# Optimization experiments

Measured on AMD Instinct MI355X. Metric: run time of the kernel, lower is better.

Reference implementation:

```python
import jax, jax.numpy as jnp
import numpy as np

WS = 7  # window size of the inner WindowAttention
EPS = 1e-5


def pc_roll(xb, shifts, axis):
    """Per-channel circular roll of [B,C,H,W] along `axis` (2 or 3).
    torch.roll semantics: out[i] = in[(i - shift) % n]."""
    n = xb.shape[axis]
    idx = (jnp.arange(n)[None, :] - shifts[:, None]) % n  # [C, n]
    if axis == 2:
        idxb = jnp.broadcast_to(idx[None, :, :, None], xb.shape)
    else:
        idxb = jnp.broadcast_to(idx[None, :, None, :], xb.shape)
    return jnp.take_along_axis(xb, idxb, axis=axis)


def layernorm(x, w, b):
    m = x.mean(-1, keepdims=True)
    v = x.var(-1, keepdims=True)
    return (x - m) * jax.lax.rsqrt(v + EPS) * w + b


def batchnorm2d(x, g, b):
    # training-mode BN: batch statistics over (B,H,W) per channel
    m = x.mean(axis=(0, 2, 3), keepdims=True)
    v = x.var(axis=(0, 2, 3), keepdims=True)
    return (x - m) * jax.lax.rsqrt(v + EPS) * g[None, :, None, None] + b[None, :, None, None]


def conv1x1(x, w, b):
    # x: [B,C,H,W], w: [Cout,Cin]
    return jnp.einsum('bchw,oc->bohw', x, w) + b[None, :, None, None]


def window_attention(q, k, v):
    # single-head Swin-style window attention, 7x7 windows, no rel-pos bias
    B, C, H, W = q.shape
    nh, nw = H // WS, W // WS

    def part(t):  # [B,C,H,W] -> [B*nh*nw, WS*WS, C]
        t = t.reshape(B, C, nh, WS, nw, WS)
        return t.transpose(0, 2, 4, 3, 5, 1).reshape(B * nh * nw, WS * WS, C)

    qw, kw, vw = part(q), part(k), part(v)
    scale = C ** -0.5
    attn = jax.nn.softmax(jnp.einsum('wnc,wmc->wnm', qw, kw) * scale, axis=-1)
    out = jnp.einsum('wnm,wmc->wnc', attn, vw)
    out = out.reshape(B, nh, nw, WS, WS, C).transpose(0, 5, 1, 3, 2, 4).reshape(B, C, H, W)
    return out


def setup_inputs() -> dict:
    B, H, W, C = 32, 56, 56, 128
    N = H * W
    key = jax.random.key(0)
    ks = jax.random.split(key, 16)
    f32 = jnp.float32

    def lin_w(k, din, dout):
        return 0.02 * jax.random.normal(k, (din, dout), dtype=f32)

    conv_std = float(np.sqrt(2.0 / C))
    inp = {
        'x': jax.random.normal(ks[0], (B, N, C), dtype=f32),
        'fc1_w': lin_w(ks[1], C, C), 'fc1_b': jnp.zeros((C,), f32),
        'fc2_w': lin_w(ks[2], C, C), 'fc2_b': jnp.zeros((C,), f32),
        'fc3_w': lin_w(ks[3], C, C), 'fc3_b': jnp.zeros((C,), f32),
        'fc4_w': lin_w(ks[4], C, C), 'fc4_b': jnp.zeros((C,), f32),
        'fc5_w': lin_w(ks[5], 2 * C, C), 'fc5_b': jnp.zeros((C,), f32),
        'fc6_w': lin_w(ks[6], 2 * C, C), 'fc6_b': jnp.zeros((C,), f32),
        'ln_w': jnp.ones((2 * C,), f32), 'ln_b': jnp.zeros((2 * C,), f32),
        'q_w': conv_std * jax.random.normal(ks[7], (C, C), dtype=f32), 'q_b': jnp.zeros((C,), f32),
        'k_w': conv_std * jax.random.normal(ks[8], (C, C), dtype=f32), 'k_b': jnp.zeros((C,), f32),
        'v_w': conv_std * jax.random.normal(ks[9], (C, C), dtype=f32), 'v_b': jnp.zeros((C,), f32),
        'bn1_g': jnp.ones((C,), f32), 'bn1_b': jnp.zeros((C,), f32),
        'bn2_g': jnp.ones((C,), f32), 'bn2_b': jnp.zeros((C,), f32),
        'H': H, 'W': W,
    }
    return inp


def reference(x, fc1_w, fc1_b, fc2_w, fc2_b, fc3_w, fc3_b, fc4_w, fc4_b,
              fc5_w, fc5_b, fc6_w, fc6_b, ln_w, ln_b,
              q_w, q_b, k_w, k_b, v_w, v_b, bn1_g, bn1_b, bn2_g, bn2_b, H, W):
    B, N, C = x.shape
    shifts = jnp.arange(C)
    gelu = lambda t: jax.nn.gelu(t, approximate=False)

    def to_bchw(t):
        return t.transpose(0, 2, 1).reshape(B, C, H, W)

    def to_bnc(t):
        return t.reshape(B, C, N).transpose(0, 2, 1)

    # branch 1: roll +c along H -> fc1 -> GELU -> roll +c along W -> fc2
    h = to_bnc(pc_roll(to_bchw(x), shifts, axis=2))
    h = gelu(h @ fc1_w + fc1_b)
    h = to_bnc(pc_roll(to_bchw(h), shifts, axis=3))
    x_1 = h @ fc2_w + fc2_b

    # branch 2: roll -c along W -> fc3 -> GELU -> roll +c along H -> fc4
    h = to_bnc(pc_roll(to_bchw(x), -shifts, axis=3))
    h = gelu(h @ fc3_w + fc3_b)
    h = to_bnc(pc_roll(to_bchw(h), shifts, axis=2))
    x_2 = h @ fc4_w + fc4_b

    x_1 = x_1 + x
    x_2 = x_2 + x
    x1 = jnp.concatenate([x_1, x_2], axis=2)          # [B,N,2C]
    x1 = layernorm(x1, ln_w, ln_b)
    x1 = x1 @ fc5_w + fc5_b
    x1 = x1 + x

    # local-attention branch (DWConv module actually runs WindowAtten + BN + ReLU)
    xb = to_bchw(x)
    att = window_attention(conv1x1(xb, q_w, q_b), conv1x1(xb, k_w, k_b), conv1x1(xb, v_w, v_b))
    x2 = jax.nn.relu(batchnorm2d(att, bn1_g, bn1_b))  # DWConv forward
    x2 = jax.nn.relu(x2)                              # act2 (idempotent, kept for fidelity)
    x2 = batchnorm2d(x2, bn2_g, bn2_b)                # norm2
    x2 = x2.reshape(B, C, N).transpose(0, 2, 1)       # [B,N,C]

    x3 = jnp.concatenate([x1, x2], axis=2)            # [B,N,2C]
    return x3 @ fc6_w + fc6_b
```

## Files before the change

### kernel.cpp

```cpp
#include <hip/hip_runtime.h>
#include <hip/hip_bf16.h>
#include <cstdint>
#include <cstddef>

typedef __bf16 bf16_t;
typedef __bf16 bf16x8 __attribute__((ext_vector_type(8)));
typedef float f32x4 __attribute__((ext_vector_type(4)));

#define B_SZ 32
#define H_SZ 56
#define W_SZ 56
#define N_TOK 3136
#define CH 128
#define M_TOT 100352

#define WOFF_FC1 0
#define WOFF_FC2 16384
#define WOFF_FC3 32768
#define WOFF_FC4 49152
#define WOFF_FC5 65536
#define WOFF_FC6 98304
#define WOFF_QW  131072
#define WOFF_KW  147456
#define WOFF_VW  163840
#define WTOT     180224

enum { A_FLAT = 0, A_WROLL, A_LN, A_BN };
enum { E_BIAS = 0, E_GELU, E_RES };

__device__ __forceinline__ float bf2f(bf16_t v) { return (float)v; }
__device__ __forceinline__ unsigned short bfbits(float v) {
    bf16_t b = (bf16_t)v; unsigned short u; __builtin_memcpy(&u, &b, 2); return u;
}

__global__ __launch_bounds__(256)
void wcvt_k(const float* __restrict__ f1, const float* __restrict__ f2,
            const float* __restrict__ f3, const float* __restrict__ f4,
            const float* __restrict__ f5, const float* __restrict__ f6,
            const float* __restrict__ qw, const float* __restrict__ kw,
            const float* __restrict__ vw, bf16_t* __restrict__ wb)
{
    const int blk = blockIdx.x;
    const int tid = threadIdx.x;
    if (blk < 32) {
        __shared__ bf16_t T[64][72];
        const float* src; bf16_t* dst; int K, t;
        if (blk < 4)       { src = f1; dst = wb + WOFF_FC1; K = 128; t = blk; }
        else if (blk < 8)  { src = f2; dst = wb + WOFF_FC2; K = 128; t = blk - 4; }
        else if (blk < 12) { src = f3; dst = wb + WOFF_FC3; K = 128; t = blk - 8; }
        else if (blk < 16) { src = f4; dst = wb + WOFF_FC4; K = 128; t = blk - 12; }
        else if (blk < 24) { src = f5; dst = wb + WOFF_FC5; K = 256; t = blk - 16; }
        else               { src = f6; dst = wb + WOFF_FC6; K = 256; t = blk - 24; }
        const int ti = t >> 1;
        const int tj = t & 1;
        for (int it = tid; it < 64 * 16; it += 256) {
            const int r = it >> 4, c4 = it & 15;
            float4 u = *(const float4*)(src + (size_t)(ti * 64 + r) * 128 + tj * 64 + c4 * 4);
            T[c4 * 4 + 0][r] = (bf16_t)u.x;
            T[c4 * 4 + 1][r] = (bf16_t)u.y;
            T[c4 * 4 + 2][r] = (bf16_t)u.z;
            T[c4 * 4 + 3][r] = (bf16_t)u.w;
        }
        __syncthreads();
        for (int it = tid; it < 64 * 8; it += 256) {
            const int n = it >> 3, ck = it & 7;
            *(uint4*)(dst + (size_t)(tj * 64 + n) * K + ti * 64 + ck * 8) =
                *(const uint4*)(&T[n][ck * 8]);
        }
    } else {
        const float* src; bf16_t* dst;
        int t = blk - 32;
        if (t < 4)      { src = qw; dst = wb + WOFF_QW; }
        else if (t < 8) { src = kw; dst = wb + WOFF_KW; t -= 4; }
        else            { src = vw; dst = wb + WOFF_VW; t -= 8; }
        const int base = t * 4096 + tid * 16;
        float4 u0 = *(const float4*)(src + base);
        float4 u1 = *(const float4*)(src + base + 4);
        float4 u2 = *(const float4*)(src + base + 8);
        float4 u3 = *(const float4*)(src + base + 12);
        bf16_t o[16] = {(bf16_t)u0.x, (bf16_t)u0.y, (bf16_t)u0.z, (bf16_t)u0.w,
                        (bf16_t)u1.x, (bf16_t)u1.y, (bf16_t)u1.z, (bf16_t)u1.w,
                        (bf16_t)u2.x, (bf16_t)u2.y, (bf16_t)u2.z, (bf16_t)u2.w,
                        (bf16_t)u3.x, (bf16_t)u3.y, (bf16_t)u3.z, (bf16_t)u3.w};
        *(uint4*)(dst + base) = *(const uint4*)o;
        *(uint4*)(dst + base + 8) = *(const uint4*)(o + 8);
    }
}

__global__ __launch_bounds__(256)
void transpose_k(const float* __restrict__ x, bf16_t* __restrict__ xT)
{
    __shared__ bf16_t T[128][70];
    const int tid = threadIdx.x;
    const int mbase = blockIdx.x * 64;
    const int bimg = mbase / N_TOK;
    const int n0 = mbase - bimg * N_TOK;
    for (int idx = tid; idx < 64 * 32; idx += 256) {
        const int tok = idx >> 5, cg = idx & 31;
        float4 u = *(const float4*)(x + (size_t)(mbase + tok) * CH + cg * 4);
        T[cg * 4 + 0][tok] = (bf16_t)u.x;
        T[cg * 4 + 1][tok] = (bf16_t)u.y;
        T[cg * 4 + 2][tok] = (bf16_t)u.z;
        T[cg * 4 + 3][tok] = (bf16_t)u.w;
    }
    __syncthreads();
    const uint* T32 = (const uint*)&T[0][0];
    for (int idx = tid; idx < 128 * 8; idx += 256) {
        const int c = idx >> 3, chunk = idx & 7;
        uint4 o;
        o.x = T32[c * 35 + chunk * 4 + 0];
        o.y = T32[c * 35 + chunk * 4 + 1];
        o.z = T32[c * 35 + chunk * 4 + 2];
        o.w = T32[c * 35 + chunk * 4 + 3];
        *(uint4*)(xT + ((size_t)(bimg * 128 + c)) * N_TOK + n0 + chunk * 8) = o;
    }
}

template<int AMODE, int KHALVES, int EPI, int WDIR, int OTRANS, int OF32>
__global__ __launch_bounds__(256)
void gemm_k(const bf16_t* __restrict__ A0, const bf16_t* __restrict__ A1,
            const bf16_t* __restrict__ Wt, const float* __restrict__ bias,
            const float* __restrict__ resid,
            const float* __restrict__ rowst,
            const float* __restrict__ lnw, const float* __restrict__ lnb,
            const float* __restrict__ bnp,
            void* __restrict__ outv)
{
    __shared__ __align__(16) char smem[17920];
    bf16_t* As = (bf16_t*)smem;
    const int tid = threadIdx.x;
    const int mbase = blockIdx.x * 64;
    const int bimg = mbase / N_TOK;
    const int n0 = mbase - bimg * N_TOK;
    const int lane = tid & 63;
    const int wv = tid >> 6;
    const int qd = lane >> 4;
    const int mr = lane & 15;
    const int KS = 128 * KHALVES;

    f32x4 acc[4][2];
#pragma unroll
    for (int i = 0; i < 4; ++i)
#pragma unroll
        for (int j = 0; j < 2; ++j) { f32x4 z = {0.f,0.f,0.f,0.f}; acc[i][j] = z; }

    for (int kh = 0; kh < KHALVES; ++kh) {
        if (kh) __syncthreads();
        if (AMODE == A_FLAT || AMODE == A_WROLL) {
            for (int idx = tid; idx < 128 * 8; idx += 256) {
                const int c = idx >> 3, chunk = idx & 7;
                const int cm = (c >= 112) ? c - 112 : (c >= 56 ? c - 56 : c);
                const bf16_t* crow = A0 + ((size_t)(bimg * 128 + c)) * N_TOK;
                if (AMODE == A_FLAT) {
                    int t = n0 + chunk * 8 + N_TOK - 56 * cm;
                    if (t >= N_TOK) t -= N_TOK;
                    uint4 u = *(const uint4*)(crow + t);
                    const bf16_t* up = (const bf16_t*)&u;
#pragma unroll
                    for (int j = 0; j < 8; ++j) As[(chunk * 8 + j) * 136 + c] = up[j];
                } else {
                    const int nl = n0 + chunk * 8;
                    const int h = nl / 56;
                    const int w0 = nl - h * 56;
                    int ws = (WDIR > 0) ? (w0 + cm) : (w0 + 56 - cm);
                    if (ws >= 56) ws -= 56;
                    const bf16_t* hrow = crow + h * 56;
                    if (ws <= 48) {
                        uint4 u = *(const uint4*)(hrow + ws);
                        const bf16_t* up = (const bf16_t*)&u;
#pragma unroll
                        for (int j = 0; j < 8; ++j) As[(chunk * 8 + j) * 136 + c] = up[j];
                    } else {
#pragma unroll
                        for (int j = 0; j < 8; ++j) {
                            int wj = ws + j; if (wj >= 56) wj -= 56;
                            As[(chunk * 8 + j) * 136 + c] = hrow[wj];
                        }
                    }
                }
            }
        } else if (AMODE == A_LN) {
            for (int idx = tid; idx < 64 * 16; idx += 256) {
                const int row = idx >> 4, ck = idx & 15;
                const int rowg = mbase + row;
                const bf16_t* src = kh ? A1 : A0;
                uint4 u = *(const uint4*)(src + (size_t)rowg * CH + ck * 8);
                const bf16_t* up = (const bf16_t*)&u;
                const float mean = rowst[2 * rowg];
                const float rstd = rowst[2 * rowg + 1];
                const int cabs = kh * 128 + ck * 8;
                bf16_t t[8];
#pragma unroll
                for (int j = 0; j < 8; ++j) {
                    float v = (bf2f(up[j]) - mean) * rstd;
                    v = v * lnw[cabs + j] + lnb[cabs + j];
                    t[j] = (bf16_t)v;
                }
                *(uint4*)(&As[row * 136 + ck * 8]) = *(const uint4*)t;
            }
        } else {
            for (int idx = tid; idx < 64 * 16; idx += 256) {
                const int row = idx >> 4, ck = idx & 15;
                const int rowg = mbase + row;
                if (kh == 0) {
                    uint4 u = *(const uint4*)(A0 + (size_t)rowg * CH + ck * 8);
                    *(uint4*)(&As[row * 136 + ck * 8]) = u;
                } else {
                    uint4 u = *(const uint4*)(A1 + (size_t)rowg * CH + ck * 8);
                    const bf16_t* up = (const bf16_t*)&u;
                    bf16_t t[8];
#pragma unroll
                    for (int j = 0; j < 8; ++j) {
                        const int c = ck * 8 + j;
                        float z = fmaxf(0.f, bf2f(up[j]) * bnp[c] + bnp[128 + c]);
                        t[j] = (bf16_t)(z * bnp[256 + c] + bnp[384 + c]);
                    }
                    *(uint4*)(&As[row * 136 + ck * 8]) = *(const uint4*)t;
                }
            }
        }
        __syncthreads();
        const bf16_t* wbase = Wt + (size_t)(wv * 32 + mr) * KS + kh * 128 + qd * 8;
        bf16x8 bfr[4][2];
#pragma unroll
        for (int kt = 0; kt < 4; ++kt)
#pragma unroll
            for (int nt = 0; nt < 2; ++nt)
                bfr[kt][nt] = *(const bf16x8*)(wbase + (size_t)(nt * 16) * KS + kt * 32);
#pragma unroll
        for (int kt = 0; kt < 4; ++kt) {
            bf16x8 af[4];
#pragma unroll
            for (int mt = 0; mt < 4; ++mt)
                af[mt] = *(const bf16x8*)(&As[(mt * 16 + mr) * 136 + kt * 32 + qd * 8]);
#pragma unroll
            for (int mt = 0; mt < 4; ++mt)
#pragma unroll
                for (int nt = 0; nt < 2; ++nt)
                    acc[mt][nt] = __builtin_amdgcn_mfma_f32_16x16x32_bf16(
                        af[mt], bfr[kt][nt], acc[mt][nt], 0, 0, 0);
        }
    }
    if (OTRANS) {
        __syncthreads();
        uint* T32 = (uint*)smem;
#pragma unroll
        for (int mt = 0; mt < 4; ++mt)
#pragma unroll
            for (int nt = 0; nt < 2; ++nt) {
                const int col = wv * 32 + nt * 16 + mr;
                const float bb = bias[col];
#pragma unroll
                for (int rp = 0; rp < 2; ++rp) {
                    float v0 = acc[mt][nt][2 * rp] + bb;
                    float v1 = acc[mt][nt][2 * rp + 1] + bb;
                    if (EPI == E_GELU) {
                        v0 = 0.5f * v0 * (1.f + erff(v0 * 0.70710678118654752f));
                        v1 = 0.5f * v1 * (1.f + erff(v1 * 0.70710678118654752f));
                    }
                    T32[col * 35 + mt * 8 + qd * 2 + rp] =
                        (uint)bfbits(v0) | ((uint)bfbits(v1) << 16);
                }
            }
        __syncthreads();
        const int c = tid >> 1, half = tid & 1;
        uint r[16];
#pragma unroll
        for (int j = 0; j < 16; ++j) r[j] = T32[c * 35 + half * 16 + j];
        bf16_t* op = (bf16_t*)outv + ((size_t)(bimg * 128 + c)) * N_TOK + n0 + half * 32;
        uint4 o0 = {r[0], r[1], r[2], r[3]};
        uint4 o1 = {r[4], r[5], r[6], r[7]};
        uint4 o2 = {r[8], r[9], r[10], r[11]};
        uint4 o3 = {r[12], r[13], r[14], r[15]};
        ((uint4*)op)[0] = o0; ((uint4*)op)[1] = o1;
        ((uint4*)op)[2] = o2; ((uint4*)op)[3] = o3;
    } else {
#pragma unroll
        for (int mt = 0; mt < 4; ++mt)
#pragma unroll
            for (int nt = 0; nt < 2; ++nt) {
                const int col = wv * 32 + nt * 16 + mr;
                const float bb = bias[col];
#pragma unroll
                for (int r = 0; r < 4; ++r) {
                    const int rowg = mbase + mt * 16 + qd * 4 + r;
                    float v = acc[mt][nt][r] + bb;
                    if (EPI == E_GELU) v = 0.5f * v * (1.f + erff(v * 0.70710678118654752f));
                    if (EPI == E_RES)  v += resid[(size_t)rowg * CH + col];
                    if (OF32) ((float*)outv)[(size_t)rowg * CH + col] = v;
                    else ((bf16_t*)outv)[(size_t)rowg * CH + col] = (bf16_t)v;
                }
            }
    }
}

__global__ __launch_bounds__(256)
void qkv_k(const float* __restrict__ x, const bf16_t* __restrict__ wb,
           const float* __restrict__ qb, const float* __restrict__ kb,
           const float* __restrict__ vb,
           bf16_t* __restrict__ qo, bf16_t* __restrict__ ko, bf16_t* __restrict__ vo)
{
    __shared__ __align__(16) bf16_t As[64 * 136];
    const int tid = threadIdx.x;
    const int mbase = blockIdx.x * 64;
    const int lane = tid & 63;
    const int wv = tid >> 6;
    const int qd = lane >> 4;
    const int mr = lane & 15;

    for (int idx = tid; idx < 64 * 16; idx += 256) {
        const int row = idx >> 4, ck = idx & 15;
        const float* p = x + (size_t)(mbase + row) * CH + ck * 8;
        float4 u0 = *(const float4*)p;
        float4 u1 = *(const float4*)(p + 4);
        bf16_t t[8] = {(bf16_t)u0.x, (bf16_t)u0.y, (bf16_t)u0.z, (bf16_t)u0.w,
                       (bf16_t)u1.x, (bf16_t)u1.y, (bf16_t)u1.z, (bf16_t)u1.w};
        *(uint4*)(&As[row * 136 + ck * 8]) = *(const uint4*)t;
    }
    __syncthreads();
    bf16x8 af[4][4];
#pragma unroll
    for (int kt = 0; kt < 4; ++kt)
#pragma unroll
        for (int mt = 0; mt < 4; ++mt)
            af[kt][mt] = *(const bf16x8*)(&As[(mt * 16 + mr) * 136 + kt * 32 + qd * 8]);

    const int woffs[3] = {WOFF_QW, WOFF_KW, WOFF_VW};
    const float* bs3[3] = {qb, kb, vb};
    bf16_t* os3[3] = {qo, ko, vo};
#pragma unroll
    for (int s = 0; s < 3; ++s) {
        const bf16_t* wbase = wb + woffs[s] + (size_t)(wv * 32 + mr) * 128 + qd * 8;
        f32x4 acc[4][2];
#pragma unroll
        for (int i = 0; i < 4; ++i)
#pragma unroll
            for (int j = 0; j < 2; ++j) { f32x4 z = {0.f,0.f,0.f,0.f}; acc[i][j] = z; }
#pragma unroll
        for (int kt = 0; kt < 4; ++kt) {
            bf16x8 bfr[2];
#pragma unroll
            for (int nt = 0; nt < 2; ++nt)
                bfr[nt] = *(const bf16x8*)(wbase + (nt * 16) * 128 + kt * 32);
#pragma unroll
            for (int mt = 0; mt < 4; ++mt)
#pragma unroll
                for (int nt = 0; nt < 2; ++nt)
                    acc[mt][nt] = __builtin_amdgcn_mfma_f32_16x16x32_bf16(
                        af[kt][mt], bfr[nt], acc[mt][nt], 0, 0, 0);
        }
        bf16_t* out = os3[s];
#pragma unroll
        for (int mt = 0; mt < 4; ++mt)
#pragma unroll
            for (int nt = 0; nt < 2; ++nt) {
                const int col = wv * 32 + nt * 16 + mr;
                const float bb = bs3[s][col];
#pragma unroll
                for (int r = 0; r < 4; ++r) {
                    const int rowg = mbase + mt * 16 + qd * 4 + r;
                    out[(size_t)rowg * CH + col] = (bf16_t)(acc[mt][nt][r] + bb);
                }
            }
    }
}

__global__ __launch_bounds__(256)
void rowstats_k(const bf16_t* __restrict__ x1p, const bf16_t* __restrict__ x2p,
                float* __restrict__ rs)
{
    const int row = blockIdx.x * 4 + (threadIdx.x >> 6);
    const int lane = threadIdx.x & 63;
    const bf16_t* p1 = x1p + (size_t)row * CH + lane * 2;
    const bf16_t* p2 = x2p + (size_t)row * CH + lane * 2;
    float a0 = bf2f(p1[0]), a1 = bf2f(p1[1]);
    float b0 = bf2f(p2[0]), b1 = bf2f(p2[1]);
    float s = a0 + a1 + b0 + b1;
    float sq = a0 * a0 + a1 * a1 + b0 * b0 + b1 * b1;
#pragma unroll
    for (int off = 32; off > 0; off >>= 1) {
        s += __shfl_down(s, off);
        sq += __shfl_down(sq, off);
    }
    if (lane == 0) {
        float mean = s * (1.f / 256.f);
        float var = sq * (1.f / 256.f) - mean * mean;
        rs[2 * row] = mean;
        rs[2 * row + 1] = rsqrtf(var + 1e-5f);
    }
}

__global__ __launch_bounds__(256, 6)
void attn_k(const bf16_t* __restrict__ qg, const bf16_t* __restrict__ kg,
            const bf16_t* __restrict__ vg, bf16_t* __restrict__ og,
            float* __restrict__ partial)
{
    __shared__ __align__(16) char smem[27136];
    bf16_t* Kr = (bf16_t*)smem;
    bf16_t* Vt = (bf16_t*)smem;
    bf16_t* Ps = (bf16_t*)(smem + 17408);
    float* bnacc = (float*)(smem + 26112);
    bf16_t* Os = (bf16_t*)smem;

    const int tid = threadIdx.x;
    const int blk = blockIdx.x;
    const int b = blk >> 6;
    const int wy = (blk >> 3) & 7;
    const int wx = blk & 7;
    const int lane = tid & 63;
    const int wv = tid >> 6;
    const int qd = lane >> 4;
    const int mr = lane & 15;

    bnacc[tid] = 0.f;

    const int kck = tid & 15;
    const int kt0 = tid >> 4;
    uint4 kld[4];
#pragma unroll
    for (int it = 0; it < 4; ++it) {
        const int i = kt0 + it * 16;
        uint4 u = {0, 0, 0, 0};
        if (i < 49) {
            const int n = (wy * 7 + i / 7) * 56 + wx * 7 + (i % 7);
            u = *(const uint4*)(kg + ((size_t)b * N_TOK + n) * CH + kck * 8);
        }
        kld[it] = u;
    }

    const int vi0 = tid & 15;
    const int vck = tid >> 4;
    uint4 vld[4];
#pragma unroll
    for (int it = 0; it < 4; ++it) {
        const int i = vi0 + it * 16;
        uint4 uv = {0, 0, 0, 0};
        if (i < 49) {
            const int n = (wy * 7 + i / 7) * 56 + wx * 7 + (i % 7);
            uv = *(const uint4*)(vg + ((size_t)b * N_TOK + n) * CH + vck * 8);
        }
        vld[it] = uv;
    }

    const int qrow = wv * 16 + mr;
    const int qc = qrow < 49 ? qrow : 48;
    const bf16_t* qptr = qg + ((size_t)b * N_TOK +
                               (wy * 7 + qc / 7) * 56 + wx * 7 + (qc % 7)) * CH + qd * 8;
    bf16x8 aq[4];
#pragma unroll
    for (int kt = 0; kt < 4; ++kt)
        aq[kt] = *(const bf16x8*)(qptr + kt * 32);

#pragma unroll
    for (int it = 0; it < 4; ++it)
        *(uint4*)(&Kr[(kt0 + it * 16) * 132 + kck * 8]) = kld[it];
    __syncthreads();

    f32x4 sacc[4];
#pragma unroll
    for (int nt = 0; nt < 4; ++nt) {
        f32x4 a = {0.f, 0.f, 0.f, 0.f};
#pragma unroll
        for (int kt = 0; kt < 4; ++kt) {
            bf16x8 bk = *(const bf16x8*)(&Kr[(nt * 16 + mr) * 132 + kt * 32 + qd * 8]);
            a = __builtin_amdgcn_mfma_f32_16x16x32_bf16(aq[kt], bk, a, 0, 0, 0);
        }
        sacc[nt] = a;
    }

    float pv[4][4];
    float inv[4];
    {
        const float SCALE = 0.088388347648318447f;
#pragma unroll
        for (int nt = 0; nt < 4; ++nt) {
            const bool bad = (nt * 16 + mr) > 48;
#pragma unroll
            for (int r = 0; r < 4; ++r)
                sacc[nt][r] = bad ? -1e30f : sacc[nt][r] * SCALE;
        }
#pragma unroll
        for (int r = 0; r < 4; ++r) {
            float m = fmaxf(fmaxf(sacc[0][r], sacc[1][r]), fmaxf(sacc[2][r], sacc[3][r]));
            m = fmaxf(m, __shfl_xor(m, 1));
            m = fmaxf(m, __shfl_xor(m, 2));
            m = fmaxf(m, __shfl_xor(m, 4));
            m = fmaxf(m, __shfl_xor(m, 8));
#pragma unroll
            for (int nt = 0; nt < 4; ++nt) pv[nt][r] = __expf(sacc[nt][r] - m);
            float s = (pv[0][r] + pv[1][r]) + (pv[2][r] + pv[3][r]);
            s += __shfl_xor(s, 1);
            s += __shfl_xor(s, 2);
            s += __shfl_xor(s, 4);
            s += __shfl_xor(s, 8);
            inv[r] = 1.f / s;
        }
    }
    __syncthreads();

#pragma unroll
    for (int it = 0; it < 4; ++it) {
        const int i = vi0 + it * 16;
        const bf16_t* vp = (const bf16_t*)&vld[it];
#pragma unroll
        for (int j = 0; j < 8; ++j)
            Vt[(vck * 8 + j) * 68 + i] = vp[j];
    }
#pragma unroll
    for (int nt = 0; nt < 4; ++nt)
#pragma unroll
        for (int r = 0; r < 4; ++r)
            Ps[(wv * 16 + qd * 4 + r) * 68 + nt * 16 + mr] = (bf16_t)(pv[nt][r] * inv[r]);
    __syncthreads();

    bf16x8 ap[2];
    ap[0] = *(const bf16x8*)(&Ps[(wv * 16 + mr) * 68 + qd * 8]);
    ap[1] = *(const bf16x8*)(&Ps[(wv * 16 + mr) * 68 + 32 + qd * 8]);
    f32x4 oacc[8];
#pragma unroll
    for (int nt = 0; nt < 8; ++nt) {
        f32x4 a = {0.f, 0.f, 0.f, 0.f};
#pragma unroll
        for (int kt = 0; kt < 2; ++kt) {
            bf16x8 bv = *(const bf16x8*)(&Vt[(nt * 16 + mr) * 68 + kt * 32 + qd * 8]);
            a = __builtin_amdgcn_mfma_f32_16x16x32_bf16(ap[kt], bv, a, 0, 0, 0);
        }
        oacc[nt] = a;
    }

#pragma unroll
    for (int nt = 0; nt < 8; ++nt) {
        const int c = nt * 16 + mr;
        float s = 0.f, sq = 0.f;
#pragma unroll
        for (int r = 0; r < 4; ++r) {
            const int q = wv * 16 + qd * 4 + r;
            if (q < 49) { const float v = oacc[nt][r]; s += v; sq += v * v; }
        }
        s += __shfl_xor(s, 16); sq += __shfl_xor(sq, 16);
        s += __shfl_xor(s, 32); sq += __shfl_xor(sq, 32);
        if (qd == 0) { atomicAdd(&bnacc[c], s); atomicAdd(&bnacc[128 + c], sq); }
    }
    __syncthreads();

#pragma unroll
    for (int nt = 0; nt < 8; ++nt) {
        const int c = nt * 16 + mr;
#pragma unroll
        for (int r = 0; r < 4; ++r) {
            const int q = wv * 16 + qd * 4 + r;
            Os[q * 136 + c] = (bf16_t)oacc[nt][r];
        }
    }
    __syncthreads();

    for (int idx = tid; idx < 49 * 16; idx += 256) {
        const int row = idx >> 4, u = idx & 15;
        const int n = (wy * 7 + row / 7) * 56 + wx * 7 + (row % 7);
        *(uint4*)(og + ((size_t)b * N_TOK + n) * CH + u * 8) =
            *(const uint4*)(&Os[row * 136 + u * 8]);
    }
    partial[(size_t)blk * 256 + tid] = bnacc[tid];
}

__global__ __launch_bounds__(256)
void bnreduce_k(const float* __restrict__ partial, float* __restrict__ accum)
{
    const int t = threadIdx.x;
    const int r0 = blockIdx.x * 16;
    float s = 0.f;
#pragma unroll
    for (int r = 0; r < 16; ++r) s += partial[(size_t)(r0 + r) * 256 + t];
    atomicAdd(&accum[t], s);
}

__global__ __launch_bounds__(256)
void bnstats2_k(const bf16_t* __restrict__ att, const float* __restrict__ g1,
                const float* __restrict__ b1, float* __restrict__ accum)
{
    __shared__ float ls[256], lq[256];
    const int c = threadIdx.x & 127;
    const int half = threadIdx.x >> 7;
    const float m = accum[c] * (1.f / (float)M_TOT);
    const float var = accum[128 + c] * (1.f / (float)M_TOT) - m * m;
    const float rstd = rsqrtf(var + 1e-5f);
    const float scl = g1[c] * rstd;
    const float sh = b1[c] - m * scl;
    const size_t rowbase = (size_t)blockIdx.x * 196;
    float s = 0.f, sq = 0.f;
    for (int r = half; r < 196; r += 2) {
        float z = fmaxf(0.f, bf2f(att[(rowbase + r) * CH + c]) * scl + sh);
        s += z; sq += z * z;
    }
    ls[threadIdx.x] = s; lq[threadIdx.x] = sq;
    __syncthreads();
    if (threadIdx.x < 128) {
        atomicAdd(&accum[256 + c], ls[threadIdx.x] + ls[threadIdx.x + 128]);
        atomicAdd(&accum[384 + c], lq[threadIdx.x] + lq[threadIdx.x + 128]);
    }
}

__global__ void bnparams_k(const float* __restrict__ accum,
                           const float* __restrict__ g1, const float* __restrict__ b1,
                           const float* __restrict__ g2, const float* __restrict__ b2,
                           float* __restrict__ bnp)
{
    const int c = threadIdx.x;
    const float inv = 1.f / (float)M_TOT;
    float m1 = accum[c] * inv;
    float v1 = accum[128 + c] * inv - m1 * m1;
    float rs1 = rsqrtf(v1 + 1e-5f);
    float s1 = g1[c] * rs1;
    float sh1 = b1[c] - m1 * s1;
    float m2 = accum[256 + c] * inv;
    float v2 = accum[384 + c] * inv - m2 * m2;
    float rs2 = rsqrtf(v2 + 1e-5f);
    float s2 = g2[c] * rs2;
    float sh2 = b2[c] - m2 * s2;
    bnp[c] = s1; bnp[128 + c] = sh1; bnp[256 + c] = s2; bnp[384 + c] = sh2;
}

__global__ void zero_k(float* __restrict__ p) { p[threadIdx.x] = 0.f; }

extern "C" void kernel_launch(void* const* d_in, const int* in_sizes, int n_in,
                              void* d_out, int out_size, void* d_ws, size_t ws_size,
                              hipStream_t stream)
{
    (void)in_sizes; (void)n_in; (void)out_size; (void)ws_size;
    const float* x     = (const float*)d_in[0];
    const float* fc1_w = (const float*)d_in[1];
    const float* fc1_b = (const float*)d_in[2];
    const float* fc2_w = (const float*)d_in[3];
    const float* fc2_b = (const float*)d_in[4];
    const float* fc3_w = (const float*)d_in[5];
    const float* fc3_b = (const float*)d_in[6];
    const float* fc4_w = (const float*)d_in[7];
    const float* fc4_b = (const float*)d_in[8];
    const float* fc5_w = (const float*)d_in[9];
    const float* fc5_b = (const float*)d_in[10];
    const float* fc6_w = (const float*)d_in[11];
    const float* fc6_b = (const float*)d_in[12];
    const float* ln_w  = (const float*)d_in[13];
    const float* ln_b  = (const float*)d_in[14];
    const float* q_w   = (const float*)d_in[15];
    const float* q_b   = (const float*)d_in[16];
    const float* k_w   = (const float*)d_in[17];
    const float* k_b   = (const float*)d_in[18];
    const float* v_w   = (const float*)d_in[19];
    const float* v_b   = (const float*)d_in[20];
    const float* bn1_g = (const float*)d_in[21];
    const float* bn1_b = (const float*)d_in[22];
    const float* bn2_g = (const float*)d_in[23];
    const float* bn2_b = (const float*)d_in[24];

    char* ws = (char*)d_ws;
    const size_t SZB = (size_t)M_TOT * CH * sizeof(bf16_t);
    bf16_t* bufA = (bf16_t*)(ws);
    bf16_t* bufB = (bf16_t*)(ws + SZB);
    bf16_t* bufC = (bf16_t*)(ws + 2 * SZB);
    bf16_t* bufD = (bf16_t*)(ws + 3 * SZB);
    float*  rs   = (float*)(ws + 4 * SZB);
    float*  accum = (float*)(ws + 4 * SZB + (size_t)M_TOT * 2 * sizeof(float));
    float*  bnp  = accum + 512;
    float*  partial = bnp + 512;
    bf16_t* wbuf = (bf16_t*)(partial + 2048 * 256);

    const dim3 blk(256);
    const int GG = M_TOT / 64;

    zero_k<<<1, 512, 0, stream>>>(accum);
    wcvt_k<<<44, blk, 0, stream>>>(fc1_w, fc2_w, fc3_w, fc4_w, fc5_w, fc6_w,
                                   q_w, k_w, v_w, wbuf);
    transpose_k<<<GG, blk, 0, stream>>>(x, bufA);
    gemm_k<A_FLAT, 1, E_GELU, 0, 1, 0><<<GG, blk, 0, stream>>>(
        bufA, nullptr, wbuf + WOFF_FC1, fc1_b, nullptr, nullptr, nullptr, nullptr, nullptr, bufB);
    gemm_k<A_WROLL, 1, E_RES, -1, 0, 0><<<GG, blk, 0, stream>>>(
        bufB, nullptr, wbuf + WOFF_FC2, fc2_b, x, nullptr, nullptr, nullptr, nullptr, bufC);
    gemm_k<A_WROLL, 1, E_GELU, 1, 1, 0><<<GG, blk, 0, stream>>>(
        bufA, nullptr, wbuf + WOFF_FC3, fc3_b, nullptr, nullptr, nullptr, nullptr, nullptr, bufB);
    gemm_k<A_FLAT, 1, E_RES, 0, 0, 0><<<GG, blk, 0, stream>>>(
        bufB, nullptr, wbuf + WOFF_FC4, fc4_b, x, nullptr, nullptr, nullptr, nullptr, bufD);
    rowstats_k<<<M_TOT / 4, blk, 0, stream>>>(bufC, bufD, rs);
    gemm_k<A_LN, 2, E_RES, 0, 0, 0><<<GG, blk, 0, stream>>>(
        bufC, bufD, wbuf + WOFF_FC5, fc5_b, x, rs, ln_w, ln_b, nullptr, bufB);
    qkv_k<<<GG, blk, 0, stream>>>(x, wbuf, q_b, k_b, v_b, bufA, bufC, bufD);
    attn_k<<<B_SZ * 64, blk, 0, stream>>>(bufA, bufC, bufD, bufA, partial);
    bnreduce_k<<<128, blk, 0, stream>>>(partial, accum);
    bnstats2_k<<<512, blk, 0, stream>>>(bufA, bn1_g, bn1_b, accum);
    bnparams_k<<<1, 128, 0, stream>>>(accum, bn1_g, bn1_b, bn2_g, bn2_b, bnp);
    gemm_k<A_BN, 2, E_BIAS, 0, 0, 1><<<GG, blk, 0, stream>>>(
        bufB, bufA, wbuf + WOFF_FC6, fc6_b, nullptr, nullptr, nullptr, nullptr, bnp, d_out);
}
```

Baseline: 467.1 us.

## Fuse fc1 and fc2 branch into one row kernel; read K directly in attention

Adds a kernel that handles one image row per block: it gathers the H-rolled input from the transposed buffer, runs fc1 with GELU into shared memory, applies the per-channel W-roll inside shared memory, then runs fc2 with bias and residual. This replaces two GEMM launches and the intermediate bufB round-trip through global memory. Separately, the attention kernel now loads K fragments straight from global memory instead of staging them in LDS, which removes one barrier and lets the V transpose overlap the softmax. The trade-off is higher LDS use per block and K loads without the staged reuse.

```diff
diff --git a/kernel.cpp b/kernel.cpp
--- a/kernel.cpp
+++ b/kernel.cpp
@@ -116,6 +116,134 @@
     }
 }
 
+__global__ __launch_bounds__(256, 4)
+void fc12_k(const bf16_t* __restrict__ xT, const float* __restrict__ x,
+            const bf16_t* __restrict__ w1, const float* __restrict__ b1,
+            const bf16_t* __restrict__ w2, const float* __restrict__ b2,
+            bf16_t* __restrict__ out)
+{
+    __shared__ __align__(16) bf16_t As[64 * 136];
+    __shared__ __align__(16) bf16_t Y[56 * 136];
+    const int tid = threadIdx.x;
+    const int blk = blockIdx.x;
+    const int bimg = blk / 56;
+    const int h = blk - bimg * 56;
+    const int nbase = h * 56;
+    const int lane = tid & 63;
+    const int wv = tid >> 6;
+    const int qd = lane >> 4;
+    const int mr = lane & 15;
+
+    for (int idx = tid; idx < 128 * 7; idx += 256) {
+        const int c = idx / 7, chunk = idx - c * 7;
+        const int cm = (c >= 112) ? c - 112 : (c >= 56 ? c - 56 : c);
+        int hs = h - cm; if (hs < 0) hs += 56;
+        const bf16_t* src = xT + ((size_t)(bimg * 128 + c)) * N_TOK + hs * 56 + chunk * 8;
+        uint4 u = *(const uint4*)src;
+        const bf16_t* up = (const bf16_t*)&u;
+#pragma unroll
+        for (int j = 0; j < 8; ++j) As[(chunk * 8 + j) * 136 + c] = up[j];
+    }
+    __syncthreads();
+
+    {
+        const bf16_t* wbase = w1 + (size_t)(wv * 32 + mr) * 128 + qd * 8;
+        bf16x8 bfr[4][2];
+#pragma unroll
+        for (int kt = 0; kt < 4; ++kt)
+#pragma unroll
+            for (int nt = 0; nt < 2; ++nt)
+                bfr[kt][nt] = *(const bf16x8*)(wbase + (size_t)(nt * 16) * 128 + kt * 32);
+        f32x4 acc[4][2];
+#pragma unroll
+        for (int i = 0; i < 4; ++i)
+#pragma unroll
+            for (int j = 0; j < 2; ++j) { f32x4 z = {0.f,0.f,0.f,0.f}; acc[i][j] = z; }
+#pragma unroll
+        for (int kt = 0; kt < 4; ++kt) {
+            bf16x8 af[4];
+#pragma unroll
+            for (int mt = 0; mt < 4; ++mt)
+                af[mt] = *(const bf16x8*)(&As[(mt * 16 + mr) * 136 + kt * 32 + qd * 8]);
+#pragma unroll
+            for (int mt = 0; mt < 4; ++mt)
+#pragma unroll
+                for (int nt = 0; nt < 2; ++nt)
+                    acc[mt][nt] = __builtin_amdgcn_mfma_f32_16x16x32_bf16(
+                        af[mt], bfr[kt][nt], acc[mt][nt], 0, 0, 0);
+        }
+#pragma unroll
+        for (int mt = 0; mt < 4; ++mt)
+#pragma unroll
+            for (int nt = 0; nt < 2; ++nt) {
+                const int col = wv * 32 + nt * 16 + mr;
+                const float bb = b1[col];
+#pragma unroll
+                for (int r = 0; r < 4; ++r) {
+                    const int row = mt * 16 + qd * 4 + r;
+                    if (row < 56) {
+                        float v = acc[mt][nt][r] + bb;
+                        v = 0.5f * v * (1.f + erff(v * 0.70710678118654752f));
+                        Y[row * 136 + col] = (bf16_t)v;
+                    }
+                }
+            }
+    }
+    __syncthreads();
+
+    for (int idx = tid; idx < 56 * 128; idx += 256) {
+        const int row = idx >> 7, c = idx & 127;
+        const int cm = (c >= 112) ? c - 112 : (c >= 56 ? c - 56 : c);
+        int ws = row - cm; if (ws < 0) ws += 56;
+        As[row * 136 + c] = Y[ws * 136 + c];
+    }
+    __syncthreads();
+
+    {
+        const bf16_t* wbase = w2 + (size_t)(wv * 32 + mr) * 128 + qd * 8;
+        bf16x8 bfr[4][2];
+#pragma unroll
+        for (int kt = 0; kt < 4; ++kt)
+#pragma unroll
+            for (int nt = 0; nt < 2; ++nt)
+                bfr[kt][nt] = *(const bf16x8*)(wbase + (size_t)(nt * 16) * 128 + kt * 32);
+        f32x4 acc[4][2];
+#pragma unroll
+        for (int i = 0; i < 4; ++i)
+#pragma unroll
+            for (int j = 0; j < 2; ++j) { f32x4 z = {0.f,0.f,0.f,0.f}; acc[i][j] = z; }
+#pragma unroll
+        for (int kt = 0; kt < 4; ++kt) {
+            bf16x8 af[4];
+#pragma unroll
+            for (int mt = 0; mt < 4; ++mt)
+                af[mt] = *(const bf16x8*)(&As[(mt * 16 + mr) * 136 + kt * 32 + qd * 8]);
+#pragma unroll
+            for (int mt = 0; mt < 4; ++mt)
+#pragma unroll
+                for (int nt = 0; nt < 2; ++nt)
+                    acc[mt][nt] = __builtin_amdgcn_mfma_f32_16x16x32_bf16(
+                        af[mt], bfr[kt][nt], acc[mt][nt], 0, 0, 0);
+        }
+#pragma unroll
+        for (int mt = 0; mt < 4; ++mt)
+#pragma unroll
+            for (int nt = 0; nt < 2; ++nt) {
+                const int col = wv * 32 + nt * 16 + mr;
+                const float bb = b2[col];
+#pragma unroll
+                for (int r = 0; r < 4; ++r) {
+                    const int row = mt * 16 + qd * 4 + r;
+                    if (row < 56) {
+                        const size_t rowg = (size_t)bimg * N_TOK + nbase + row;
+                        float v = acc[mt][nt][r] + bb + x[rowg * CH + col];
+                        out[rowg * CH + col] = (bf16_t)v;
+                    }
+                }
+            }
+    }
+}
+
 template<int AMODE, int KHALVES, int EPI, int WDIR, int OTRANS, int OF32>
 __global__ __launch_bounds__(256)
 void gemm_k(const bf16_t* __restrict__ A0, const bf16_t* __restrict__ A1,
@@ -396,7 +524,6 @@
             float* __restrict__ partial)
 {
     __shared__ __align__(16) char smem[27136];
-    bf16_t* Kr = (bf16_t*)smem;
     bf16_t* Vt = (bf16_t*)smem;
     bf16_t* Ps = (bf16_t*)(smem + 17408);
     float* bnacc = (float*)(smem + 26112);
@@ -414,20 +541,6 @@
 
     bnacc[tid] = 0.f;
 
-    const int kck = tid & 15;
-    const int kt0 = tid >> 4;
-    uint4 kld[4];
-#pragma unroll
-    for (int it = 0; it < 4; ++it) {
-        const int i = kt0 + it * 16;
-        uint4 u = {0, 0, 0, 0};
-        if (i < 49) {
-            const int n = (wy * 7 + i / 7) * 56 + wx * 7 + (i % 7);
-            u = *(const uint4*)(kg + ((size_t)b * N_TOK + n) * CH + kck * 8);
-        }
-        kld[it] = u;
-    }
-
     const int vi0 = tid & 15;
     const int vck = tid >> 4;
     uint4 vld[4];
@@ -451,25 +564,31 @@
     for (int kt = 0; kt < 4; ++kt)
         aq[kt] = *(const bf16x8*)(qptr + kt * 32);
 
-#pragma unroll
-    for (int it = 0; it < 4; ++it)
-        *(uint4*)(&Kr[(kt0 + it * 16) * 132 + kck * 8]) = kld[it];
-    __syncthreads();
-
     f32x4 sacc[4];
 #pragma unroll
     for (int nt = 0; nt < 4; ++nt) {
+        const int krow = nt * 16 + mr;
+        const int kc = krow < 49 ? krow : 48;
+        const bf16_t* kptr = kg + ((size_t)b * N_TOK +
+                                   (wy * 7 + kc / 7) * 56 + wx * 7 + (kc % 7)) * CH + qd * 8;
         f32x4 a = {0.f, 0.f, 0.f, 0.f};
 #pragma unroll
         for (int kt = 0; kt < 4; ++kt) {
-            bf16x8 bk = *(const bf16x8*)(&Kr[(nt * 16 + mr) * 132 + kt * 32 + qd * 8]);
+            bf16x8 bk = *(const bf16x8*)(kptr + kt * 32);
             a = __builtin_amdgcn_mfma_f32_16x16x32_bf16(aq[kt], bk, a, 0, 0, 0);
         }
         sacc[nt] = a;
     }
 
-    float pv[4][4];
-    float inv[4];
+#pragma unroll
+    for (int it = 0; it < 4; ++it) {
+        const int i = vi0 + it * 16;
+        const bf16_t* vp = (const bf16_t*)&vld[it];
+#pragma unroll
+        for (int j = 0; j < 8; ++j)
+            Vt[(vck * 8 + j) * 68 + i] = vp[j];
+    }
+
     {
         const float SCALE = 0.088388347648318447f;
 #pragma unroll
@@ -479,6 +598,8 @@
             for (int r = 0; r < 4; ++r)
                 sacc[nt][r] = bad ? -1e30f : sacc[nt][r] * SCALE;
         }
+        float pv[4][4];
+        float inv[4];
 #pragma unroll
         for (int r = 0; r < 4; ++r) {
             float m = fmaxf(fmaxf(sacc[0][r], sacc[1][r]), fmaxf(sacc[2][r], sacc[3][r]));
@@ -495,22 +616,12 @@
             s += __shfl_xor(s, 8);
             inv[r] = 1.f / s;
         }
-    }
-    __syncthreads();
-
-#pragma unroll
-    for (int it = 0; it < 4; ++it) {
-        const int i = vi0 + it * 16;
-        const bf16_t* vp = (const bf16_t*)&vld[it];
-#pragma unroll
-        for (int j = 0; j < 8; ++j)
-            Vt[(vck * 8 + j) * 68 + i] = vp[j];
-    }
-#pragma unroll
-    for (int nt = 0; nt < 4; ++nt)
-#pragma unroll
-        for (int r = 0; r < 4; ++r)
-            Ps[(wv * 16 + qd * 4 + r) * 68 + nt * 16 + mr] = (bf16_t)(pv[nt][r] * inv[r]);
+#pragma unroll
+        for (int nt = 0; nt < 4; ++nt)
+#pragma unroll
+            for (int r = 0; r < 4; ++r)
+                Ps[(wv * 16 + qd * 4 + r) * 68 + nt * 16 + mr] = (bf16_t)(pv[nt][r] * inv[r]);
+    }
     __syncthreads();
 
     bf16x8 ap[2];
@@ -672,10 +783,8 @@
     wcvt_k<<<44, blk, 0, stream>>>(fc1_w, fc2_w, fc3_w, fc4_w, fc5_w, fc6_w,
                                    q_w, k_w, v_w, wbuf);
     transpose_k<<<GG, blk, 0, stream>>>(x, bufA);
-    gemm_k<A_FLAT, 1, E_GELU, 0, 1, 0><<<GG, blk, 0, stream>>>(
-        bufA, nullptr, wbuf + WOFF_FC1, fc1_b, nullptr, nullptr, nullptr, nullptr, nullptr, bufB);
-    gemm_k<A_WROLL, 1, E_RES, -1, 0, 0><<<GG, blk, 0, stream>>>(
-        bufB, nullptr, wbuf + WOFF_FC2, fc2_b, x, nullptr, nullptr, nullptr, nullptr, bufC);
+    fc12_k<<<B_SZ * 56, blk, 0, stream>>>(
+        bufA, x, wbuf + WOFF_FC1, fc1_b, wbuf + WOFF_FC2, fc2_b, bufC);
     gemm_k<A_WROLL, 1, E_GELU, 1, 1, 0><<<GG, blk, 0, stream>>>(
         bufA, nullptr, wbuf + WOFF_FC3, fc3_b, nullptr, nullptr, nullptr, nullptr, nullptr, bufB);
     gemm_k<A_FLAT, 1, E_RES, 0, 0, 0><<<GG, blk, 0, stream>>>(
```

After: 443.3 us. -5.1%, faster.
